# Performance work log

Measured on AMD Instinct MI355X. Metric: run time of the kernel, lower is better.

## Reference

```python
import jax, jax.numpy as jnp
import numpy as np

B, N, T, D, H, K = 16, 512, 64, 64, 8, 3
DK = D // H  # 8


def setup_inputs() -> dict:
    key = jax.random.key(0)
    ks = jax.random.split(key, 12)
    f = lambda k, s: jax.random.normal(k, s, dtype=jnp.float32)
    return {
        "query": f(ks[0], (B, N, T, D)),
        "key": f(ks[1], (B, N, T, D)),
        "value": f(ks[2], (B, N, T, D)),
        "att": jnp.zeros((1,), jnp.float32),  # unused: original's att bias always resolves to 0
        "mask": jax.random.randint(ks[3], (B, T, T), 0, 2).astype(jnp.int32),
        "Wq": f(ks[4], (D, D, 1, K)) * 0.1, "bq": f(ks[5], (D,)) * 0.1,
        "Wk": f(ks[6], (D, D, 1, K)) * 0.1, "bk": f(ks[7], (D,)) * 0.1,
        "Wv": f(ks[8], (D, D)) * 0.1, "bv": f(ks[9], (D,)) * 0.1,
        "Wo": f(ks[10], (D, D)) * 0.1, "bo": f(ks[11], (D,)) * 0.1,
    }


def _causal_conv(x, w, b):
    # x: (B,N,T,D); Conv2d over (N,T) with kernel (1,K), left-pad K-1 on T == causal conv
    xc = jnp.transpose(x, (0, 3, 1, 2))  # (B,D,N,T)
    y = jax.lax.conv_general_dilated(
        xc, w, window_strides=(1, 1), padding=((0, 0), (K - 1, 0)),
        dimension_numbers=("NCHW", "OIHW", "NCHW"))
    y = y + b[None, :, None, None]
    # (B,D,N,T) -> view (B,H,DK,N,T) -> permute to (B,N,H,T,DK)
    y = y.reshape(B, H, DK, N, T)
    return jnp.transpose(y, (0, 3, 1, 4, 2))


def reference(query, key, value, att, mask, Wq, bq, Wk, bk, Wv, bv, Wo, bo):
    q = _causal_conv(query, Wq, bq)                    # (B,N,H,T,DK)
    k = _causal_conv(key, Wk, bk)                      # (B,N,H,T,DK)
    v = (value @ Wv.T + bv).reshape(B, N, T, H, DK)
    v = jnp.transpose(v, (0, 1, 3, 2, 4))              # (B,N,H,T,DK)

    scores = jnp.einsum("bnhtd,bnhsd->bnhts", q, k) / jnp.sqrt(jnp.float32(DK))
    # NOTE: original adds `att` bias but the try/except always yields att=0
    m = mask[:, None, None, :, :]                      # (B,1,1,T,T)
    scores = jnp.where(m == 0, jnp.float32(-1e9), scores)
    p = jax.nn.softmax(scores, axis=-1)                # (B,N,H,T,T); dropout p=0.0 -> identity

    x = jnp.einsum("bnhts,bnhsd->bnhtd", p, v)         # (B,N,H,T,DK)
    x = jnp.transpose(x, (0, 1, 3, 2, 4)).reshape(B, N, T, D)
    return x @ Wo.T + bo, p
```

## Files before the change

### kernel.cpp

```cpp
#include <hip/hip_runtime.h>


#define OUT_ELEMS 33554432ull

typedef unsigned short u16;
typedef unsigned int u32;
typedef __attribute__((ext_vector_type(8))) short short8;
typedef __attribute__((ext_vector_type(4))) float f32x4;

__device__ __forceinline__ u16 f2b(float f) {
  u32 u = __float_as_uint(f);
  return (u16)((u + 0x7fffu + ((u >> 16) & 1u)) >> 16);
}

__global__ __launch_bounds__(256) void prep_weights(
    const float* __restrict__ Wq, const float* __restrict__ Wk,
    const float* __restrict__ Wv, const float* __restrict__ Wo,
    u16* __restrict__ ws) {
  int i = blockIdx.x * 256 + threadIdx.x;
  int lane = (i >> 3) & 63;
  int e = i & 7;
  int m15 = lane & 15, g = lane >> 4;
  if (i < 12288) {
    int f = i >> 9;
    int j = f >> 3, kk = (f >> 2) & 1, nt = f & 3;
    int d = nt * 16 + m15, c = kk * 32 + g * 8 + e;
    ws[i] = f2b(Wq[(d * 64 + c) * 3 + j]);
  } else if (i < 24576) {
    int f = (i - 12288) >> 9;
    int j = f >> 3, kk = (f >> 2) & 1, nt = f & 3;
    int d = nt * 16 + m15, c = kk * 32 + g * 8 + e;
    ws[i] = f2b(Wk[(d * 64 + c) * 3 + j]);
  } else if (i < 28672) {
    int f = (i - 24576) >> 9;
    int w = f >> 1, kk = f & 1;
    int d = 16 * w + m15, c = kk * 32 + g * 8 + e;
    ws[i] = f2b(Wv[d * 64 + c]);
  } else if (i < 32768) {
    int f = (i - 28672) >> 9;
    int kk = f >> 2, nt = f & 3;
    int dp = nt * 16 + m15, c = kk * 32 + g * 8 + e;
    ws[i] = f2b(Wo[dp * 64 + c]);
  }
}

__global__ __launch_bounds__(256, 3) void fused_attn(
    const float* __restrict__ q_in, const float* __restrict__ k_in,
    const float* __restrict__ v_in, const int* __restrict__ mask,
    const u16* __restrict__ ws,
    const float* __restrict__ bq, const float* __restrict__ bk,
    const float* __restrict__ bv, const float* __restrict__ bo,
    float* __restrict__ out, float* __restrict__ p_out) {
  __shared__ __align__(16) u16 xb[66 * 72];
  __shared__ __align__(16) u16 qb[64 * 72];
  __shared__ __align__(16) u16 kb[64 * 72];
  __shared__ __align__(16) u16 vT[64 * 72];
  __shared__ __align__(16) u16 xo[64 * 72];

  const int tid = threadIdx.x;
  const int bid = blockIdx.x;
  const int b = bid >> 9;
  const int l = tid & 63;
  const int w = tid >> 6;
  const int g = l >> 4;
  const int m15 = l & 15;

  const u16* wsq = ws;
  const u16* wsk = ws + 12288;
  const u16* wsv = ws + 24576;
  const u16* wso = ws + 28672;

  const short8 z8 = {0, 0, 0, 0, 0, 0, 0, 0};

  if (tid < 72) ((u32*)xb)[tid] = 0u;

  auto stage = [&](const float* __restrict__ src) {
#pragma unroll
    for (int cc = 0; cc < 2; cc++) {
      int c = tid * 2 + cc;
      const float* p = src + c * 8;
      float4 x0 = *(const float4*)(p);
      float4 x1 = *(const float4*)(p + 4);
      u32 p0 = (u32)f2b(x0.x) | ((u32)f2b(x0.y) << 16);
      u32 p1 = (u32)f2b(x0.z) | ((u32)f2b(x0.w) << 16);
      u32 p2 = (u32)f2b(x1.x) | ((u32)f2b(x1.y) << 16);
      u32 p3 = (u32)f2b(x1.z) | ((u32)f2b(x1.w) << 16);
      int r = c >> 3, k8 = (c & 7) * 8;
      *(uint4*)(xb + (r + 2) * 72 + k8) = make_uint4(p0, p1, p2, p3);
    }
  };

  auto conv = [&](const u16* __restrict__ wpack, const float* __restrict__ bias,
                  float scale, u16* __restrict__ dst) {
    f32x4 acc[4];
#pragma unroll
    for (int nt = 0; nt < 4; nt++) {
      float bb = bias[nt * 16 + m15];
      acc[nt] = (f32x4){bb, bb, bb, bb};
    }
#pragma unroll
    for (int j = 0; j < 3; j++) {
#pragma unroll
      for (int kk = 0; kk < 2; kk++) {
        short8 a = *(const short8*)(xb + (16 * w + m15 + j) * 72 + kk * 32 + g * 8);
#pragma unroll
        for (int nt = 0; nt < 4; nt++) {
          short8 bf = *(const short8*)(wpack + (size_t)((j * 2 + kk) * 4 + nt) * 512 + l * 8);
          acc[nt] = __builtin_amdgcn_mfma_f32_16x16x32_bf16(a, bf, acc[nt], 0, 0, 0);
        }
      }
    }
#pragma unroll
    for (int nt = 0; nt < 4; nt++)
#pragma unroll
      for (int r = 0; r < 4; r++)
        dst[(16 * w + g * 4 + r) * 72 + nt * 16 + m15] = f2b(acc[nt][r] * scale);
  };

  stage(q_in + (size_t)bid * 4096);
  __syncthreads();
  conv(wsq, bq, 0.35355339059327373f, qb);
  __syncthreads();

  stage(k_in + (size_t)bid * 4096);
  __syncthreads();
  conv(wsk, bk, 1.0f, kb);
  __syncthreads();

  stage(v_in + (size_t)bid * 4096);
  __syncthreads();
  {
    f32x4 acc[4];
    float bm0 = bv[16 * w + g * 4 + 0], bm1 = bv[16 * w + g * 4 + 1];
    float bm2 = bv[16 * w + g * 4 + 2], bm3 = bv[16 * w + g * 4 + 3];
#pragma unroll
    for (int nt = 0; nt < 4; nt++) acc[nt] = (f32x4){bm0, bm1, bm2, bm3};
#pragma unroll
    for (int kk = 0; kk < 2; kk++) {
      short8 a = *(const short8*)(wsv + (size_t)(w * 2 + kk) * 512 + l * 8);
#pragma unroll
      for (int nt = 0; nt < 4; nt++) {
        short8 bf = *(const short8*)(xb + (nt * 16 + m15 + 2) * 72 + kk * 32 + g * 8);
        acc[nt] = __builtin_amdgcn_mfma_f32_16x16x32_bf16(a, bf, acc[nt], 0, 0, 0);
      }
    }
#pragma unroll
    for (int nt = 0; nt < 4; nt++)
#pragma unroll
      for (int r = 0; r < 4; r++)
        vT[(16 * w + g * 4 + r) * 72 + nt * 16 + m15] = f2b(acc[nt][r]);
  }

  u32 mb = 0;
#pragma unroll
  for (int nt = 0; nt < 4; nt++)
#pragma unroll
    for (int r = 0; r < 4; r++)
      if (mask[(size_t)b * 4096 + (16 * w + g * 4 + r) * 64 + nt * 16 + m15])
        mb |= 1u << (nt * 4 + r);
  __syncthreads();

  u16* pb = xb;

#pragma unroll 1
  for (int h = 0; h < 8; h++) {
    short8 aq = *(const short8*)(qb + (16 * w + m15) * 72 + h * 8);
    if (g != 0) aq = z8;
    f32x4 s4[4];
#pragma unroll
    for (int nt = 0; nt < 4; nt++) {
      short8 bk8 = *(const short8*)(kb + (nt * 16 + m15) * 72 + h * 8);
      if (g != 0) bk8 = z8;
      f32x4 zero = {0.f, 0.f, 0.f, 0.f};
      s4[nt] = __builtin_amdgcn_mfma_f32_16x16x32_bf16(aq, bk8, zero, 0, 0, 0);
    }
    float e[4][4];
    float rs0 = 0.f, rs1 = 0.f, rs2 = 0.f, rs3 = 0.f;
#pragma unroll
    for (int nt = 0; nt < 4; nt++) {
      e[nt][0] = (mb & (1u << (nt * 4 + 0))) ? __expf(s4[nt][0]) : 0.f;
      e[nt][1] = (mb & (1u << (nt * 4 + 1))) ? __expf(s4[nt][1]) : 0.f;
      e[nt][2] = (mb & (1u << (nt * 4 + 2))) ? __expf(s4[nt][2]) : 0.f;
      e[nt][3] = (mb & (1u << (nt * 4 + 3))) ? __expf(s4[nt][3]) : 0.f;
      rs0 += e[nt][0]; rs1 += e[nt][1]; rs2 += e[nt][2]; rs3 += e[nt][3];
    }
#pragma unroll
    for (int off = 1; off <= 8; off <<= 1) {
      rs0 += __shfl_xor(rs0, off);
      rs1 += __shfl_xor(rs1, off);
      rs2 += __shfl_xor(rs2, off);
      rs3 += __shfl_xor(rs3, off);
    }
    float ri0 = __fdividef(1.f, rs0 + 1e-30f);
    float ri1 = __fdividef(1.f, rs1 + 1e-30f);
    float ri2 = __fdividef(1.f, rs2 + 1e-30f);
    float ri3 = __fdividef(1.f, rs3 + 1e-30f);
    float* pg = p_out + (((size_t)bid * 8 + h) * 4096);
#pragma unroll
    for (int nt = 0; nt < 4; nt++) {
      float p0 = e[nt][0] * ri0, p1 = e[nt][1] * ri1;
      float p2 = e[nt][2] * ri2, p3 = e[nt][3] * ri3;
      pg[(16 * w + g * 4 + 0) * 64 + nt * 16 + m15] = p0;
      pg[(16 * w + g * 4 + 1) * 64 + nt * 16 + m15] = p1;
      pg[(16 * w + g * 4 + 2) * 64 + nt * 16 + m15] = p2;
      pg[(16 * w + g * 4 + 3) * 64 + nt * 16 + m15] = p3;
      pb[(16 * w + g * 4 + 0) * 72 + nt * 16 + m15] = f2b(p0);
      pb[(16 * w + g * 4 + 1) * 72 + nt * 16 + m15] = f2b(p1);
      pb[(16 * w + g * 4 + 2) * 72 + nt * 16 + m15] = f2b(p2);
      pb[(16 * w + g * 4 + 3) * 72 + nt * 16 + m15] = f2b(p3);
    }
    f32x4 xacc = {0.f, 0.f, 0.f, 0.f};
#pragma unroll
    for (int kk = 0; kk < 2; kk++) {
      short8 ap = *(const short8*)(pb + (16 * w + m15) * 72 + kk * 32 + g * 8);
      short8 bv8 = *(const short8*)(vT + (h * 8 + (m15 & 7)) * 72 + kk * 32 + g * 8);
      xacc = __builtin_amdgcn_mfma_f32_16x16x32_bf16(ap, bv8, xacc, 0, 0, 0);
    }
    if (m15 < 8) {
#pragma unroll
      for (int r = 0; r < 4; r++)
        xo[(16 * w + g * 4 + r) * 72 + h * 8 + m15] = f2b(xacc[r]);
    }
  }

  {
    f32x4 acc[4];
#pragma unroll
    for (int nt = 0; nt < 4; nt++) {
      float bb = bo[nt * 16 + m15];
      acc[nt] = (f32x4){bb, bb, bb, bb};
    }
#pragma unroll
    for (int kk = 0; kk < 2; kk++) {
      short8 ax = *(const short8*)(xo + (16 * w + m15) * 72 + kk * 32 + g * 8);
#pragma unroll
      for (int nt = 0; nt < 4; nt++) {
        short8 bf = *(const short8*)(wso + (size_t)(kk * 4 + nt) * 512 + l * 8);
        acc[nt] = __builtin_amdgcn_mfma_f32_16x16x32_bf16(ax, bf, acc[nt], 0, 0, 0);
      }
    }
#pragma unroll
    for (int nt = 0; nt < 4; nt++)
#pragma unroll
      for (int r = 0; r < 4; r++)
        out[(size_t)bid * 4096 + (16 * w + g * 4 + r) * 64 + nt * 16 + m15] = acc[nt][r];
  }
}

extern "C" void kernel_launch(void* const* d_in, const int* in_sizes, int n_in,
                              void* d_out, int out_size, void* d_ws, size_t ws_size,
                              hipStream_t stream) {
  const float* query = (const float*)d_in[0];
  const float* key   = (const float*)d_in[1];
  const float* value = (const float*)d_in[2];
  const int*   mask  = (const int*)d_in[4];
  const float* Wq = (const float*)d_in[5];
  const float* bq = (const float*)d_in[6];
  const float* Wk = (const float*)d_in[7];
  const float* bk = (const float*)d_in[8];
  const float* Wv = (const float*)d_in[9];
  const float* bv = (const float*)d_in[10];
  const float* Wo = (const float*)d_in[11];
  const float* bo = (const float*)d_in[12];

  float* out = (float*)d_out;
  float* p_out = out + OUT_ELEMS;
  u16* ws = (u16*)d_ws;

  hipLaunchKernelGGL(prep_weights, dim3(128), dim3(256), 0, stream,
                     Wq, Wk, Wv, Wo, ws);
  hipLaunchKernelGGL(fused_attn, dim3(8192), dim3(256), 0, stream,
                     query, key, value, mask, ws, bq, bk, bv, bo, out, p_out);
}
```

Before: 321.4 us.

## Swap MFMA operand roles so each lane owns a row for vectorized stores

Swaps the A/B operands of the conv, QK^T and output-projection MFMAs so the accumulator is transposed: each lane now holds four consecutive columns of one row. This lets the P, output and LDS writes use float4/uint2 vector stores instead of scattered scalar stores, and makes the softmax row sum a two-step cross-lane reduction instead of four four-step shuffles. The mask is packed once into a shared bitmask using int4 loads. The main target is the store traffic for the large P output, at the cost of an extra small shared buffer and a changed register layout.

```diff
diff --git a/kernel.cpp b/kernel.cpp
--- a/kernel.cpp
+++ b/kernel.cpp
@@ -5,6 +5,7 @@
 
 typedef unsigned short u16;
 typedef unsigned int u32;
+typedef unsigned long long u64;
 typedef __attribute__((ext_vector_type(8))) short short8;
 typedef __attribute__((ext_vector_type(4))) float f32x4;
 
@@ -56,6 +57,7 @@
   __shared__ __align__(16) u16 kb[64 * 72];
   __shared__ __align__(16) u16 vT[64 * 72];
   __shared__ __align__(16) u16 xo[64 * 72];
+  __shared__ __align__(16) u16 mskw[256];
 
   const int tid = threadIdx.x;
   const int bid = blockIdx.x;
@@ -71,6 +73,7 @@
   const u16* wso = ws + 28672;
 
   const short8 z8 = {0, 0, 0, 0, 0, 0, 0, 0};
+  const int rowt = 16 * w + m15;
 
   if (tid < 72) ((u32*)xb)[tid] = 0u;
 
@@ -94,39 +97,38 @@
                   float scale, u16* __restrict__ dst) {
     f32x4 acc[4];
 #pragma unroll
-    for (int nt = 0; nt < 4; nt++) {
-      float bb = bias[nt * 16 + m15];
-      acc[nt] = (f32x4){bb, bb, bb, bb};
+    for (int sb = 0; sb < 4; sb++) {
+      float4 bb = *(const float4*)(bias + sb * 16 + g * 4);
+      acc[sb] = (f32x4){bb.x, bb.y, bb.z, bb.w};
     }
 #pragma unroll
     for (int j = 0; j < 3; j++) {
 #pragma unroll
       for (int kk = 0; kk < 2; kk++) {
-        short8 a = *(const short8*)(xb + (16 * w + m15 + j) * 72 + kk * 32 + g * 8);
-#pragma unroll
-        for (int nt = 0; nt < 4; nt++) {
-          short8 bf = *(const short8*)(wpack + (size_t)((j * 2 + kk) * 4 + nt) * 512 + l * 8);
-          acc[nt] = __builtin_amdgcn_mfma_f32_16x16x32_bf16(a, bf, acc[nt], 0, 0, 0);
+        short8 xf = *(const short8*)(xb + (rowt + j) * 72 + kk * 32 + g * 8);
+#pragma unroll
+        for (int sb = 0; sb < 4; sb++) {
+          short8 wf = *(const short8*)(wpack + (size_t)((j * 2 + kk) * 4 + sb) * 512 + l * 8);
+          acc[sb] = __builtin_amdgcn_mfma_f32_16x16x32_bf16(wf, xf, acc[sb], 0, 0, 0);
         }
       }
     }
 #pragma unroll
-    for (int nt = 0; nt < 4; nt++)
-#pragma unroll
-      for (int r = 0; r < 4; r++)
-        dst[(16 * w + g * 4 + r) * 72 + nt * 16 + m15] = f2b(acc[nt][r] * scale);
+    for (int sb = 0; sb < 4; sb++) {
+      u32 lo = (u32)f2b(acc[sb][0] * scale) | ((u32)f2b(acc[sb][1] * scale) << 16);
+      u32 hi = (u32)f2b(acc[sb][2] * scale) | ((u32)f2b(acc[sb][3] * scale) << 16);
+      *(uint2*)(dst + rowt * 72 + sb * 16 + g * 4) = make_uint2(lo, hi);
+    }
   };
 
   stage(q_in + (size_t)bid * 4096);
   __syncthreads();
   conv(wsq, bq, 0.35355339059327373f, qb);
   __syncthreads();
-
   stage(k_in + (size_t)bid * 4096);
   __syncthreads();
   conv(wsk, bk, 1.0f, kb);
   __syncthreads();
-
   stage(v_in + (size_t)bid * 4096);
   __syncthreads();
   {
@@ -151,68 +153,62 @@
         vT[(16 * w + g * 4 + r) * 72 + nt * 16 + m15] = f2b(acc[nt][r]);
   }
 
-  u32 mb = 0;
-#pragma unroll
-  for (int nt = 0; nt < 4; nt++)
-#pragma unroll
-    for (int r = 0; r < 4; r++)
-      if (mask[(size_t)b * 4096 + (16 * w + g * 4 + r) * 64 + nt * 16 + m15])
-        mb |= 1u << (nt * 4 + r);
+  {
+    int row = tid >> 2, qt = tid & 3;
+    const int* mp = mask + (size_t)b * 4096 + row * 64 + qt * 16;
+    u32 bits = 0;
+#pragma unroll
+    for (int i4 = 0; i4 < 4; i4++) {
+      int4 mv = *(const int4*)(mp + i4 * 4);
+      bits |= ((u32)mv.x << (i4 * 4)) | ((u32)mv.y << (i4 * 4 + 1)) |
+              ((u32)mv.z << (i4 * 4 + 2)) | ((u32)mv.w << (i4 * 4 + 3));
+    }
+    mskw[row * 4 + qt] = (u16)bits;
+  }
   __syncthreads();
 
   u16* pb = xb;
+  const u64 mg = ((const u64*)mskw)[rowt] >> (g * 4);
+  const int t64 = rowt * 64;
 
 #pragma unroll 1
   for (int h = 0; h < 8; h++) {
-    short8 aq = *(const short8*)(qb + (16 * w + m15) * 72 + h * 8);
-    if (g != 0) aq = z8;
+    short8 bq8 = *(const short8*)(qb + rowt * 72 + h * 8);
+    if (g != 0) bq8 = z8;
     f32x4 s4[4];
 #pragma unroll
-    for (int nt = 0; nt < 4; nt++) {
-      short8 bk8 = *(const short8*)(kb + (nt * 16 + m15) * 72 + h * 8);
-      if (g != 0) bk8 = z8;
+    for (int sb = 0; sb < 4; sb++) {
+      short8 ak = *(const short8*)(kb + (sb * 16 + m15) * 72 + h * 8);
+      if (g != 0) ak = z8;
       f32x4 zero = {0.f, 0.f, 0.f, 0.f};
-      s4[nt] = __builtin_amdgcn_mfma_f32_16x16x32_bf16(aq, bk8, zero, 0, 0, 0);
+      s4[sb] = __builtin_amdgcn_mfma_f32_16x16x32_bf16(ak, bq8, zero, 0, 0, 0);
     }
     float e[4][4];
-    float rs0 = 0.f, rs1 = 0.f, rs2 = 0.f, rs3 = 0.f;
-#pragma unroll
-    for (int nt = 0; nt < 4; nt++) {
-      e[nt][0] = (mb & (1u << (nt * 4 + 0))) ? __expf(s4[nt][0]) : 0.f;
-      e[nt][1] = (mb & (1u << (nt * 4 + 1))) ? __expf(s4[nt][1]) : 0.f;
-      e[nt][2] = (mb & (1u << (nt * 4 + 2))) ? __expf(s4[nt][2]) : 0.f;
-      e[nt][3] = (mb & (1u << (nt * 4 + 3))) ? __expf(s4[nt][3]) : 0.f;
-      rs0 += e[nt][0]; rs1 += e[nt][1]; rs2 += e[nt][2]; rs3 += e[nt][3];
-    }
-#pragma unroll
-    for (int off = 1; off <= 8; off <<= 1) {
-      rs0 += __shfl_xor(rs0, off);
-      rs1 += __shfl_xor(rs1, off);
-      rs2 += __shfl_xor(rs2, off);
-      rs3 += __shfl_xor(rs3, off);
-    }
-    float ri0 = __fdividef(1.f, rs0 + 1e-30f);
-    float ri1 = __fdividef(1.f, rs1 + 1e-30f);
-    float ri2 = __fdividef(1.f, rs2 + 1e-30f);
-    float ri3 = __fdividef(1.f, rs3 + 1e-30f);
-    float* pg = p_out + (((size_t)bid * 8 + h) * 4096);
-#pragma unroll
-    for (int nt = 0; nt < 4; nt++) {
-      float p0 = e[nt][0] * ri0, p1 = e[nt][1] * ri1;
-      float p2 = e[nt][2] * ri2, p3 = e[nt][3] * ri3;
-      pg[(16 * w + g * 4 + 0) * 64 + nt * 16 + m15] = p0;
-      pg[(16 * w + g * 4 + 1) * 64 + nt * 16 + m15] = p1;
-      pg[(16 * w + g * 4 + 2) * 64 + nt * 16 + m15] = p2;
-      pg[(16 * w + g * 4 + 3) * 64 + nt * 16 + m15] = p3;
-      pb[(16 * w + g * 4 + 0) * 72 + nt * 16 + m15] = f2b(p0);
-      pb[(16 * w + g * 4 + 1) * 72 + nt * 16 + m15] = f2b(p1);
-      pb[(16 * w + g * 4 + 2) * 72 + nt * 16 + m15] = f2b(p2);
-      pb[(16 * w + g * 4 + 3) * 72 + nt * 16 + m15] = f2b(p3);
+    float rs = 0.f;
+#pragma unroll
+    for (int sb = 0; sb < 4; sb++)
+#pragma unroll
+      for (int r = 0; r < 4; r++) {
+        float v = ((mg >> (sb * 16 + r)) & 1ull) ? __expf(s4[sb][r]) : 0.f;
+        e[sb][r] = v;
+        rs += v;
+      }
+    rs += __shfl_xor(rs, 16);
+    rs += __shfl_xor(rs, 32);
+    float ri = __fdividef(1.f, rs + 1e-30f);
+    float* pg = p_out + ((size_t)bid * 8 + h) * 4096 + t64;
+#pragma unroll
+    for (int sb = 0; sb < 4; sb++) {
+      float4 pv = make_float4(e[sb][0] * ri, e[sb][1] * ri, e[sb][2] * ri, e[sb][3] * ri);
+      *(float4*)(pg + sb * 16 + g * 4) = pv;
+      u32 lo = (u32)f2b(pv.x) | ((u32)f2b(pv.y) << 16);
+      u32 hi = (u32)f2b(pv.z) | ((u32)f2b(pv.w) << 16);
+      *(uint2*)(pb + rowt * 72 + sb * 16 + g * 4) = make_uint2(lo, hi);
     }
     f32x4 xacc = {0.f, 0.f, 0.f, 0.f};
 #pragma unroll
     for (int kk = 0; kk < 2; kk++) {
-      short8 ap = *(const short8*)(pb + (16 * w + m15) * 72 + kk * 32 + g * 8);
+      short8 ap = *(const short8*)(pb + rowt * 72 + kk * 32 + g * 8);
       short8 bv8 = *(const short8*)(vT + (h * 8 + (m15 & 7)) * 72 + kk * 32 + g * 8);
       xacc = __builtin_amdgcn_mfma_f32_16x16x32_bf16(ap, bv8, xacc, 0, 0, 0);
     }
@@ -226,24 +222,23 @@
   {
     f32x4 acc[4];
 #pragma unroll
-    for (int nt = 0; nt < 4; nt++) {
-      float bb = bo[nt * 16 + m15];
-      acc[nt] = (f32x4){bb, bb, bb, bb};
+    for (int sb = 0; sb < 4; sb++) {
+      float4 bb = *(const float4*)(bo + sb * 16 + g * 4);
+      acc[sb] = (f32x4){bb.x, bb.y, bb.z, bb.w};
     }
 #pragma unroll
     for (int kk = 0; kk < 2; kk++) {
-      short8 ax = *(const short8*)(xo + (16 * w + m15) * 72 + kk * 32 + g * 8);
-#pragma unroll
-      for (int nt = 0; nt < 4; nt++) {
-        short8 bf = *(const short8*)(wso + (size_t)(kk * 4 + nt) * 512 + l * 8);
-        acc[nt] = __builtin_amdgcn_mfma_f32_16x16x32_bf16(ax, bf, acc[nt], 0, 0, 0);
-      }
-    }
-#pragma unroll
-    for (int nt = 0; nt < 4; nt++)
-#pragma unroll
-      for (int r = 0; r < 4; r++)
-        out[(size_t)bid * 4096 + (16 * w + g * 4 + r) * 64 + nt * 16 + m15] = acc[nt][r];
+      short8 xf = *(const short8*)(xo + rowt * 72 + kk * 32 + g * 8);
+#pragma unroll
+      for (int sb = 0; sb < 4; sb++) {
+        short8 wf = *(const short8*)(wso + (size_t)(kk * 4 + sb) * 512 + l * 8);
+        acc[sb] = __builtin_amdgcn_mfma_f32_16x16x32_bf16(wf, xf, acc[sb], 0, 0, 0);
+      }
+    }
+    float* ob = out + (size_t)bid * 4096 + t64;
+#pragma unroll
+    for (int sb = 0; sb < 4; sb++)
+      *(float4*)(ob + sb * 16 + g * 4) = make_float4(acc[sb][0], acc[sb][1], acc[sb][2], acc[sb][3]);
   }
 }
 
```

New measurement: 343.4 us. +6.8%, slower.
